# Kernel optimization log

Hardware: AMD Instinct MI355X
Metric: run time of the kernel (lower is better)

Reference implementation:

```python
import jax, jax.numpy as jnp
import numpy as np

NF, D, H = 32, 256, 128  # n_features, d_model, d_model//2
B, T = 16, 512
EPS = 1e-5

def _ln(x, g, b):
    m = jnp.mean(x, axis=-1, keepdims=True)
    v = jnp.mean((x - m) ** 2, axis=-1, keepdims=True)
    return (x - m) * jax.lax.rsqrt(v + EPS) * g + b


def setup_inputs() -> dict:
    key = jax.random.key(0)
    ks = jax.random.split(key, 16)
    s = 0.05
    inp = {
        "x": jax.random.normal(ks[0], (B, T, NF), dtype=jnp.float32),
        # batched per-feature GRN params (d_in=1 -> fc1 weight is (NF,H))
        "w1": jax.random.normal(ks[1], (NF, H)) * s,
        "b1": jnp.zeros((NF, H)),
        "w2": jax.random.normal(ks[2], (NF, H, D)) * s,
        "b2": jnp.zeros((NF, D)),
        "wg": jax.random.normal(ks[3], (NF, H, D)) * s,
        "bg": jnp.zeros((NF, D)),
        "ws": jax.random.normal(ks[4], (NF, D)) * s,  # skip Linear(1,D)
        "bs": jnp.zeros((NF, D)),
        "ln_g": jnp.ones((NF, D)),
        "ln_b": jnp.zeros((NF, D)),
        # weight GRN: d_in=NF*D, d_hidden=D, d_out=NF
        "W1": jax.random.normal(ks[5], (NF * D, D)) * s,
        "B1": jnp.zeros((D,)),
        "W2": jax.random.normal(ks[6], (D, NF)) * s,
        "B2": jnp.zeros((NF,)),
        "Wg": jax.random.normal(ks[7], (D, NF)) * s,
        "Bg": jnp.zeros((NF,)),
        "Ws": jax.random.normal(ks[8], (NF * D, NF)) * s,
        "Bs": jnp.zeros((NF,)),
        "LN_g": jnp.ones((NF,)),
        "LN_b": jnp.zeros((NF,)),
    }
    return inp


def reference(x, w1, b1, w2, b2, wg, bg, ws, bs, ln_g, ln_b,
              W1, B1, W2, B2, Wg, Bg, Ws, Bs, LN_g, LN_b):
    Bn, Tn, Fn = x.shape
    # --- all per-feature GRNs batched over the feature axis (dropout=eval/identity) ---
    h = jax.nn.elu(x[..., None] * w1 + b1)                      # (B,T,F,H)
    proj = jnp.einsum('btfh,fhd->btfd', h, w2) + b2             # (B,T,F,D)
    gate = jax.nn.sigmoid(jnp.einsum('btfh,fhd->btfd', h, wg) + bg)
    skip = x[..., None] * ws + bs                               # (B,T,F,D)
    stacked = _ln(skip + gate * proj, ln_g, ln_b)               # (B,T,F,D)
    # --- softmax feature weights from mean-pooled flat features ---
    flat_pooled = stacked.mean(axis=1).reshape(Bn, Fn * stacked.shape[-1])  # (B,F*D)
    hw = jax.nn.elu(flat_pooled @ W1 + B1)                      # (B,D)
    pw = hw @ W2 + B2
    gw = jax.nn.sigmoid(hw @ Wg + Bg)
    wgrn = _ln(flat_pooled @ Ws + Bs + gw * pw, LN_g, LN_b)     # (B,F)
    weights = jax.nn.softmax(wgrn, axis=-1)                     # (B,F)
    # --- weighted feature combine ---
    selected = jnp.einsum('btfd,bf->btd', stacked, weights)     # (B,T,D)
    return selected, weights
```

## Files before the change

kernel.cpp:

```cpp
#include <hip/hip_runtime.h>
#include <hip/hip_fp16.h>

#define NF 32
#define DM 256
#define HH 128
#define BB 16
#define TT 512
#define BT 8192
#define OUT_W_OFF 2097152
#define EPS 1e-5f

typedef __bf16 bf16x8 __attribute__((ext_vector_type(8)));
typedef float  f32x16 __attribute__((ext_vector_type(16)));
typedef __fp16 f16x2 __attribute__((ext_vector_type(2)));
typedef __fp16 f16x8 __attribute__((ext_vector_type(8)));

__device__ __forceinline__ float eluf(float z){ return z > 0.f ? z : __expf(z) - 1.f; }
__device__ __forceinline__ float sigm(float z){ return 1.f/(1.f + __expf(-z)); }
__device__ __forceinline__ unsigned f2bf(float x){
  unsigned u = __float_as_uint(x);
  u += 0x7fffu + ((u>>16)&1u);
  return u>>16;
}
__device__ __forceinline__ float rdlane(float v, int l){
  return __uint_as_float(__builtin_amdgcn_readlane(__float_as_uint(v), l));
}
__device__ __forceinline__ float qsel(float v, int mb, int lane){
  float a0 = rdlane(v, mb), a1 = rdlane(v, mb+4);
  return (lane & 32) ? a1 : a0;
}

template<int MT>
__device__ __forceinline__ void build_A(uint4* Apack, const float* __restrict__ x,
                                        const float* __restrict__ w1, const float* __restrict__ b1,
                                        int f, int tok0, int tid){
  #pragma unroll
  for (int p = 0; p < MT*2; ++p){
    int slot = tid + p*256;
    int l  = slot & 63;
    int ks = (slot>>6)&7;
    int mt = slot>>9;
    int m  = mt*32 + (l&31);
    int k0 = ks*16 + (l>>5)*8;
    float xv = x[(tok0+m)*NF + f];
    const float* wp = w1 + f*HH + k0;
    const float* bp = b1 + f*HH + k0;
    float4 wa = *(const float4*)wp, wb = *(const float4*)(wp+4);
    float4 ba = *(const float4*)bp, bb = *(const float4*)(bp+4);
    float h0 = eluf(fmaf(xv, wa.x, ba.x));
    float h1 = eluf(fmaf(xv, wa.y, ba.y));
    float h2 = eluf(fmaf(xv, wa.z, ba.z));
    float h3 = eluf(fmaf(xv, wa.w, ba.w));
    float h4 = eluf(fmaf(xv, wb.x, bb.x));
    float h5 = eluf(fmaf(xv, wb.y, bb.y));
    float h6 = eluf(fmaf(xv, wb.z, bb.z));
    float h7 = eluf(fmaf(xv, wb.w, bb.w));
    uint4 pk;
    pk.x = f2bf(h0) | (f2bf(h1)<<16);
    pk.y = f2bf(h2) | (f2bf(h3)<<16);
    pk.z = f2bf(h4) | (f2bf(h5)<<16);
    pk.w = f2bf(h6) | (f2bf(h7)<<16);
    Apack[slot] = pk;
  }
}

__global__ __launch_bounds__(256) void k_prep(const float* __restrict__ w2,
                                              const float* __restrict__ wgm,
                                              uint4* __restrict__ Wpk){
  __shared__ float ssrc[2][128][32];
  const int tid = threadIdx.x;
  const int f = blockIdx.x, c = blockIdx.y;
  #pragma unroll
  for (int it = 0; it < 32; ++it){
    int idx = tid + it*256;
    int arr = idx >> 12;
    int rem = idx & 4095;
    int k = rem >> 5, dd = rem & 31;
    const float* src = arr ? wgm : w2;
    ssrc[arr][k][dd] = src[(f*HH + k)*DM + c*32 + dd];
  }
  __syncthreads();
  #pragma unroll
  for (int p = 0; p < 4; ++p){
    int oc = tid + p*256;
    int nt = oc>>9, ks = (oc>>6)&7, l = oc&63;
    int k0 = ks*16 + (l>>5)*8, dd = l&31;
    float v[8];
    #pragma unroll
    for (int j=0;j<8;++j) v[j] = ssrc[nt][k0+j][dd];
    uint4 pk;
    pk.x = f2bf(v[0]) | (f2bf(v[1])<<16);
    pk.y = f2bf(v[2]) | (f2bf(v[3])<<16);
    pk.z = f2bf(v[4]) | (f2bf(v[5])<<16);
    pk.w = f2bf(v[6]) | (f2bf(v[7])<<16);
    Wpk[(f*8 + c)*1024 + oc] = pk;
  }
}

__global__ __launch_bounds__(256) void k_pass1(const float* __restrict__ x,  const float* __restrict__ w1,
    const float* __restrict__ b1, const float* __restrict__ b2, const float* __restrict__ bg,
    const float* __restrict__ wsk, const float* __restrict__ bsk,
    const float* __restrict__ lng, const float* __restrict__ lnb,
    const uint4* __restrict__ Wpk,
    float* __restrict__ pooled, uint4* __restrict__ stk4){
  __shared__ uint4 smem[4096];
  __shared__ float muL[128], rsL[128];
  __shared__ float poolbuf[256];
  const int tid = threadIdx.x, lane = tid&63, wid = tid>>6;
  const int col = lane&31, q = lane>>5;
  const int f = blockIdx.y;
  const int tok0 = blockIdx.x*128;
  const int b = tok0 >> 9;
  poolbuf[tid] = 0.f;
  build_A<4>(smem, x, w1, b1, f, tok0, tid);
  __syncthreads();
  bf16x8 afr[8];
  #pragma unroll
  for (int ks=0; ks<8; ++ks) afr[ks] = __builtin_bit_cast(bf16x8, smem[(wid*8+ks)*64 + lane]);
  float xl = x[(tok0 + wid*32 + col)*NF + f];
  float xr[16];
  #pragma unroll
  for (int r=0;r<16;++r) xr[r] = qsel(xl, (r&3)+8*(r>>2), lane);
  __syncthreads();
  __fp16* stage = (__fp16*)smem;
  float sum[16], ssq[16];
  #pragma unroll
  for (int r=0;r<16;++r){ sum[r]=0.f; ssq[r]=0.f; }
  for (int c=0; c<8; ++c){
    const uint4* wb = Wpk + (f*8 + c)*1024;
    bf16x8 bf0[8], bf1[8];
    #pragma unroll
    for (int ks=0;ks<8;++ks) bf0[ks] = __builtin_bit_cast(bf16x8, wb[ks*64 + lane]);
    #pragma unroll
    for (int ks=0;ks<8;++ks) bf1[ks] = __builtin_bit_cast(bf16x8, wb[512 + ks*64 + lane]);
    f32x16 acc0 = {0.f}, acc1 = {0.f};
    #pragma unroll
    for (int ks=0;ks<8;++ks){
      acc0 = __builtin_amdgcn_mfma_f32_32x32x16_bf16(afr[ks], bf0[ks], acc0, 0,0,0);
      acc1 = __builtin_amdgcn_mfma_f32_32x32x16_bf16(afr[ks], bf1[ks], acc1, 0,0,0);
    }
    const int d = c*32 + col;
    const float b2v = b2[f*DM+d], bgv = bg[f*DM+d];
    const float wsv = wsk[f*DM+d], bsv = bsk[f*DM+d];
    #pragma unroll
    for (int i=0;i<8;++i){
      const int r0 = 2*i, r1 = 2*i+1;
      const int m0 = (r0&3) + 8*(i>>1) + 4*q;
      const int t0 = wid*32 + m0;
      float sv0 = fmaf(xr[r0], wsv, bsv) + sigm(acc1[r0]+bgv)*(acc0[r0]+b2v);
      float sv1 = fmaf(xr[r1], wsv, bsv) + sigm(acc1[r1]+bgv)*(acc0[r1]+b2v);
      sum[r0] += sv0; ssq[r0] = fmaf(sv0, sv0, ssq[r0]);
      sum[r1] += sv1; ssq[r1] = fmaf(sv1, sv1, ssq[r1]);
      stage[ t0   *256 + d] = (__fp16)sv0;
      stage[(t0+1)*256 + d] = (__fp16)sv1;
    }
  }
  #pragma unroll
  for (int r=0;r<16;++r){
    float s1 = sum[r], s2 = ssq[r];
    s1 += __shfl_xor(s1,1);  s2 += __shfl_xor(s2,1);
    s1 += __shfl_xor(s1,2);  s2 += __shfl_xor(s2,2);
    s1 += __shfl_xor(s1,4);  s2 += __shfl_xor(s2,4);
    s1 += __shfl_xor(s1,8);  s2 += __shfl_xor(s2,8);
    s1 += __shfl_xor(s1,16); s2 += __shfl_xor(s2,16);
    float mu = s1 * (1.f/256.f);
    float var = fmaf(-mu, mu, s2*(1.f/256.f));
    sum[r] = mu;
    ssq[r] = rsqrtf(fmaxf(var, 0.f) + EPS);
  }
  if (col == 0){
    #pragma unroll
    for (int r=0;r<16;++r){
      int m = (r&3) + 8*(r>>2) + 4*q;
      muL[wid*32 + m] = sum[r];
      rsL[wid*32 + m] = ssq[r];
    }
  }
  __syncthreads();
  const int oc = tid & 31;
  float4 ga = *(const float4*)(lng + f*DM + oc*8);
  float4 gb = *(const float4*)(lng + f*DM + oc*8 + 4);
  float4 ba = *(const float4*)(lnb + f*DM + oc*8);
  float4 bb = *(const float4*)(lnb + f*DM + oc*8 + 4);
  float gj[8] = {ga.x,ga.y,ga.z,ga.w,gb.x,gb.y,gb.z,gb.w};
  float bj[8] = {ba.x,ba.y,ba.z,ba.w,bb.x,bb.y,bb.z,bb.w};
  float ps[8];
  #pragma unroll
  for (int j=0;j<8;++j) ps[j]=0.f;
  #pragma unroll
  for (int p=0;p<16;++p){
    int slot = tid + p*256;
    int t = slot >> 5;
    uint4 v = smem[slot];
    f16x8 s8 = __builtin_bit_cast(f16x8, v);
    float mu = muL[t], rs = rsL[t];
    float nmr = -mu*rs;
    float sh[8];
    #pragma unroll
    for (int j=0;j<8;++j){
      sh[j] = fmaf(fmaf((float)s8[j], rs, nmr), gj[j], bj[j]);
      ps[j] += sh[j];
    }
    uint4 pk;
    pk.x = __builtin_bit_cast(unsigned, __builtin_amdgcn_cvt_pkrtz(sh[0], sh[1]));
    pk.y = __builtin_bit_cast(unsigned, __builtin_amdgcn_cvt_pkrtz(sh[2], sh[3]));
    pk.z = __builtin_bit_cast(unsigned, __builtin_amdgcn_cvt_pkrtz(sh[4], sh[5]));
    pk.w = __builtin_bit_cast(unsigned, __builtin_amdgcn_cvt_pkrtz(sh[6], sh[7]));
    stk4[(size_t)f*262144 + (size_t)(tok0 + t)*32 + oc] = pk;
  }
  #pragma unroll
  for (int j=0;j<8;++j) atomicAdd(&poolbuf[oc*8 + j], ps[j]);
  __syncthreads();
  atomicAdd(&pooled[b*8192 + f*DM + tid], poolbuf[tid]);
}

__global__ __launch_bounds__(256) void k_pass2a(const float* __restrict__ pooled,
    const float* __restrict__ W1, const float* __restrict__ Wsm,
    float* __restrict__ hw_pre, float* __restrict__ sk_pre){
  __shared__ float fl[512];
  const int tid = threadIdx.x;
  const int b = blockIdx.x;
  const int k0 = blockIdx.y * 512;
  fl[tid]       = pooled[b*8192 + k0 + tid]       * (1.f/512.f);
  fl[tid+256]   = pooled[b*8192 + k0 + tid + 256] * (1.f/512.f);
  __syncthreads();
  float acc = 0.f;
  const float* wcol = W1 + (size_t)k0*DM + tid;
  #pragma unroll 4
  for (int i=0;i<512;++i) acc = fmaf(fl[i], wcol[(size_t)i*DM], acc);
  atomicAdd(&hw_pre[b*DM + tid], acc);
  const int colj = tid & 31, sub = tid >> 5;
  float acc2 = 0.f;
  const float* wscol = Wsm + (size_t)(k0 + sub*64)*NF + colj;
  const float* fls = fl + sub*64;
  #pragma unroll 4
  for (int i=0;i<64;++i) acc2 = fmaf(fls[i], wscol[(size_t)i*NF], acc2);
  atomicAdd(&sk_pre[b*NF + colj], acc2);
}

__global__ __launch_bounds__(64) void k_pass2b(const float* __restrict__ hw_pre, const float* __restrict__ sk_pre,
    const float* __restrict__ B1, const float* __restrict__ W2, const float* __restrict__ B2,
    const float* __restrict__ Wg, const float* __restrict__ Bg, const float* __restrict__ Bs,
    const float* __restrict__ LNg, const float* __restrict__ LNb,
    float* __restrict__ out, float* __restrict__ wsel){
  __shared__ float hw[256];
  const int tid = threadIdx.x, b = blockIdx.x;
  for (int i=tid;i<256;i+=64) hw[i] = eluf(hw_pre[b*DM+i] + B1[i]);
  __syncthreads();
  if (tid < 32){
    const int j = tid;
    float ap = B2[j], ag = Bg[j];
    #pragma unroll 4
    for (int i=0;i<256;++i){ float h = hw[i]; ap = fmaf(h, W2[i*NF+j], ap); ag = fmaf(h, Wg[i*NF+j], ag); }
    float gw = sigm(ag);
    float v = sk_pre[b*NF+j] + Bs[j] + gw*ap;
    float s1 = v;
    s1 += __shfl_xor(s1,1); s1 += __shfl_xor(s1,2); s1 += __shfl_xor(s1,4); s1 += __shfl_xor(s1,8); s1 += __shfl_xor(s1,16);
    float mean = s1*(1.f/32.f);
    float dv = v - mean;
    float s2 = dv*dv;
    s2 += __shfl_xor(s2,1); s2 += __shfl_xor(s2,2); s2 += __shfl_xor(s2,4); s2 += __shfl_xor(s2,8); s2 += __shfl_xor(s2,16);
    float wn = fmaf(dv * rsqrtf(s2*(1.f/32.f) + EPS), LNg[j], LNb[j]);
    float mx = wn;
    mx = fmaxf(mx, __shfl_xor(mx,1)); mx = fmaxf(mx, __shfl_xor(mx,2)); mx = fmaxf(mx, __shfl_xor(mx,4));
    mx = fmaxf(mx, __shfl_xor(mx,8)); mx = fmaxf(mx, __shfl_xor(mx,16));
    float e = __expf(wn - mx);
    float se = e;
    se += __shfl_xor(se,1); se += __shfl_xor(se,2); se += __shfl_xor(se,4); se += __shfl_xor(se,8); se += __shfl_xor(se,16);
    float wgt = e / se;
    out[OUT_W_OFF + b*NF + j] = wgt;
    wsel[b*NF + j] = wgt;
  }
}

__global__ __launch_bounds__(256) void k_comb(const uint4* __restrict__ stk4,
    const float* __restrict__ wsel, float* __restrict__ out){
  __shared__ float wloc[NF];
  const int tid = threadIdx.x, lane = tid&63;
  const int t = blockIdx.x*4 + (tid>>6);
  const int b = t >> 9;
  if (tid < NF) wloc[tid] = wsel[b*NF + tid];
  __syncthreads();
  const int oc = lane&31, fh = lane>>5;
  float acc[8];
  #pragma unroll
  for (int j=0;j<8;++j) acc[j]=0.f;
  #pragma unroll
  for (int j=0;j<16;++j){
    int f = fh*16 + j;
    uint4 v = stk4[(size_t)f*262144 + (size_t)t*32 + oc];
    f16x8 hv = __builtin_bit_cast(f16x8, v);
    float wf = wloc[f];
    #pragma unroll
    for (int jj=0;jj<8;++jj) acc[jj] = fmaf(wf, (float)hv[jj], acc[jj]);
  }
  #pragma unroll
  for (int jj=0;jj<8;++jj) acc[jj] += __shfl_xor(acc[jj], 32);
  if (fh == 0){
    float4* o = (float4*)(out + (size_t)t*DM + oc*8);
    o[0] = make_float4(acc[0],acc[1],acc[2],acc[3]);
    o[1] = make_float4(acc[4],acc[5],acc[6],acc[7]);
  }
}

extern "C" void kernel_launch(void* const* d_in, const int* in_sizes, int n_in,
                              void* d_out, int out_size, void* d_ws, size_t ws_size,
                              hipStream_t stream) {
  const float* x   = (const float*)d_in[0];
  const float* w1  = (const float*)d_in[1];
  const float* b1  = (const float*)d_in[2];
  const float* w2  = (const float*)d_in[3];
  const float* b2  = (const float*)d_in[4];
  const float* wgm = (const float*)d_in[5];
  const float* bg  = (const float*)d_in[6];
  const float* wsk = (const float*)d_in[7];
  const float* bsk = (const float*)d_in[8];
  const float* lng = (const float*)d_in[9];
  const float* lnb = (const float*)d_in[10];
  const float* W1  = (const float*)d_in[11];
  const float* B1  = (const float*)d_in[12];
  const float* W2  = (const float*)d_in[13];
  const float* B2  = (const float*)d_in[14];
  const float* Wg  = (const float*)d_in[15];
  const float* Bg  = (const float*)d_in[16];
  const float* Wsm = (const float*)d_in[17];
  const float* Bs  = (const float*)d_in[18];
  const float* LNg = (const float*)d_in[19];
  const float* LNb = (const float*)d_in[20];
  float* out = (float*)d_out;

  char* ws = (char*)d_ws;
  uint4* Wpk    = (uint4*)ws;
  uint4* stk4   = (uint4*)(ws + 4194304);
  float* pooled = (float*)(ws + 138412032);
  float* hw_pre = (float*)(ws + 138936320);
  float* sk_pre = (float*)(ws + 138952704);
  float* wsel   = (float*)(ws + 138954752);

  (void)hipMemsetAsync(pooled, 0, 524288, stream);
  (void)hipMemsetAsync(hw_pre, 0, 16384 + 2048, stream);

  k_prep<<<dim3(32,8), 256, 0, stream>>>(w2, wgm, Wpk);
  k_pass1<<<dim3(64,32), 256, 0, stream>>>(x, w1, b1, b2, bg, wsk, bsk, lng, lnb,
                                           Wpk, pooled, stk4);
  k_pass2a<<<dim3(16,16), 256, 0, stream>>>(pooled, W1, Wsm, hw_pre, sk_pre);
  k_pass2b<<<16, 64, 0, stream>>>(hw_pre, sk_pre, B1, W2, B2, Wg, Bg, Bs, LNg, LNb, out, wsel);
  k_comb<<<2048, 256, 0, stream>>>(stk4, wsel, out);
}
```

Measured before the change: 321.0 us.

## Store un-normalized pre-LN values and defer LayerNorm into pooling and combine

k_pass1 now builds the ELU hidden fragments directly in registers instead of staging them through shared memory. It writes raw pre-LayerNorm fp16 values straight to global memory in MFMA fragment order, along with per-token mean and rstd arrays. Pooling is computed algebraically from these raw values plus the statistics, removing the shared-memory LN pass and its extra syncs. k_comb applies gamma, beta, mean and rstd on the fly while reducing over features, at the cost of more per-element arithmetic, a shared-memory transpose and a more complex fragment-order layout.

```diff
diff --git a/kernel.cpp b/kernel.cpp
--- a/kernel.cpp
+++ b/kernel.cpp
@@ -30,40 +30,6 @@
   return (lane & 32) ? a1 : a0;
 }
 
-template<int MT>
-__device__ __forceinline__ void build_A(uint4* Apack, const float* __restrict__ x,
-                                        const float* __restrict__ w1, const float* __restrict__ b1,
-                                        int f, int tok0, int tid){
-  #pragma unroll
-  for (int p = 0; p < MT*2; ++p){
-    int slot = tid + p*256;
-    int l  = slot & 63;
-    int ks = (slot>>6)&7;
-    int mt = slot>>9;
-    int m  = mt*32 + (l&31);
-    int k0 = ks*16 + (l>>5)*8;
-    float xv = x[(tok0+m)*NF + f];
-    const float* wp = w1 + f*HH + k0;
-    const float* bp = b1 + f*HH + k0;
-    float4 wa = *(const float4*)wp, wb = *(const float4*)(wp+4);
-    float4 ba = *(const float4*)bp, bb = *(const float4*)(bp+4);
-    float h0 = eluf(fmaf(xv, wa.x, ba.x));
-    float h1 = eluf(fmaf(xv, wa.y, ba.y));
-    float h2 = eluf(fmaf(xv, wa.z, ba.z));
-    float h3 = eluf(fmaf(xv, wa.w, ba.w));
-    float h4 = eluf(fmaf(xv, wb.x, bb.x));
-    float h5 = eluf(fmaf(xv, wb.y, bb.y));
-    float h6 = eluf(fmaf(xv, wb.z, bb.z));
-    float h7 = eluf(fmaf(xv, wb.w, bb.w));
-    uint4 pk;
-    pk.x = f2bf(h0) | (f2bf(h1)<<16);
-    pk.y = f2bf(h2) | (f2bf(h3)<<16);
-    pk.z = f2bf(h4) | (f2bf(h5)<<16);
-    pk.w = f2bf(h6) | (f2bf(h7)<<16);
-    Apack[slot] = pk;
-  }
-}
-
 __global__ __launch_bounds__(256) void k_prep(const float* __restrict__ w2,
                                               const float* __restrict__ wgm,
                                               uint4* __restrict__ Wpk){
@@ -97,42 +63,66 @@
   }
 }
 
-__global__ __launch_bounds__(256) void k_pass1(const float* __restrict__ x,  const float* __restrict__ w1,
-    const float* __restrict__ b1, const float* __restrict__ b2, const float* __restrict__ bg,
+__global__ __launch_bounds__(256) void k_pass1(
+    const float* __restrict__ x,  const float* __restrict__ w1, const float* __restrict__ b1,
+    const float* __restrict__ b2, const float* __restrict__ bg,
     const float* __restrict__ wsk, const float* __restrict__ bsk,
     const float* __restrict__ lng, const float* __restrict__ lnb,
     const uint4* __restrict__ Wpk,
+    float* __restrict__ muw, float* __restrict__ rsw,
     float* __restrict__ pooled, uint4* __restrict__ stk4){
-  __shared__ uint4 smem[4096];
-  __shared__ float muL[128], rsL[128];
   __shared__ float poolbuf[256];
+  __shared__ float Cbuf;
   const int tid = threadIdx.x, lane = tid&63, wid = tid>>6;
   const int col = lane&31, q = lane>>5;
   const int f = blockIdx.y;
   const int tok0 = blockIdx.x*128;
   const int b = tok0 >> 9;
   poolbuf[tid] = 0.f;
-  build_A<4>(smem, x, w1, b1, f, tok0, tid);
-  __syncthreads();
+  if (tid == 0) Cbuf = 0.f;
+  __syncthreads();
+  const float xl = x[(tok0 + wid*32 + col)*NF + f];
   bf16x8 afr[8];
-  #pragma unroll
-  for (int ks=0; ks<8; ++ks) afr[ks] = __builtin_bit_cast(bf16x8, smem[(wid*8+ks)*64 + lane]);
-  float xl = x[(tok0 + wid*32 + col)*NF + f];
+  {
+    const float* wp = w1 + f*HH + q*8;
+    const float* bp = b1 + f*HH + q*8;
+    #pragma unroll
+    for (int ks=0;ks<8;++ks){
+      float4 wa = *(const float4*)(wp + ks*16);
+      float4 wb = *(const float4*)(wp + ks*16 + 4);
+      float4 ba = *(const float4*)(bp + ks*16);
+      float4 bb = *(const float4*)(bp + ks*16 + 4);
+      float h0 = eluf(fmaf(xl, wa.x, ba.x));
+      float h1 = eluf(fmaf(xl, wa.y, ba.y));
+      float h2 = eluf(fmaf(xl, wa.z, ba.z));
+      float h3 = eluf(fmaf(xl, wa.w, ba.w));
+      float h4 = eluf(fmaf(xl, wb.x, bb.x));
+      float h5 = eluf(fmaf(xl, wb.y, bb.y));
+      float h6 = eluf(fmaf(xl, wb.z, bb.z));
+      float h7 = eluf(fmaf(xl, wb.w, bb.w));
+      uint4 pk;
+      pk.x = f2bf(h0) | (f2bf(h1)<<16);
+      pk.y = f2bf(h2) | (f2bf(h3)<<16);
+      pk.z = f2bf(h4) | (f2bf(h5)<<16);
+      pk.w = f2bf(h6) | (f2bf(h7)<<16);
+      afr[ks] = __builtin_bit_cast(bf16x8, pk);
+    }
+  }
   float xr[16];
   #pragma unroll
   for (int r=0;r<16;++r) xr[r] = qsel(xl, (r&3)+8*(r>>2), lane);
-  __syncthreads();
-  __fp16* stage = (__fp16*)smem;
   float sum[16], ssq[16];
   #pragma unroll
   for (int r=0;r<16;++r){ sum[r]=0.f; ssq[r]=0.f; }
+  const size_t sbase = (size_t)f*262144 + (size_t)blockIdx.x*4096
+                     + (size_t)(wid*128 + q*64 + col*2);
   for (int c=0; c<8; ++c){
-    const uint4* wb = Wpk + (f*8 + c)*1024;
+    const uint4* wb4 = Wpk + (f*8 + c)*1024;
     bf16x8 bf0[8], bf1[8];
     #pragma unroll
-    for (int ks=0;ks<8;++ks) bf0[ks] = __builtin_bit_cast(bf16x8, wb[ks*64 + lane]);
-    #pragma unroll
-    for (int ks=0;ks<8;++ks) bf1[ks] = __builtin_bit_cast(bf16x8, wb[512 + ks*64 + lane]);
+    for (int ks=0;ks<8;++ks) bf0[ks] = __builtin_bit_cast(bf16x8, wb4[ks*64 + lane]);
+    #pragma unroll
+    for (int ks=0;ks<8;++ks) bf1[ks] = __builtin_bit_cast(bf16x8, wb4[512 + ks*64 + lane]);
     f32x16 acc0 = {0.f}, acc1 = {0.f};
     #pragma unroll
     for (int ks=0;ks<8;++ks){
@@ -142,18 +132,21 @@
     const int d = c*32 + col;
     const float b2v = b2[f*DM+d], bgv = bg[f*DM+d];
     const float wsv = wsk[f*DM+d], bsv = bsk[f*DM+d];
+    unsigned pk[8];
     #pragma unroll
     for (int i=0;i<8;++i){
       const int r0 = 2*i, r1 = 2*i+1;
-      const int m0 = (r0&3) + 8*(i>>1) + 4*q;
-      const int t0 = wid*32 + m0;
       float sv0 = fmaf(xr[r0], wsv, bsv) + sigm(acc1[r0]+bgv)*(acc0[r0]+b2v);
       float sv1 = fmaf(xr[r1], wsv, bsv) + sigm(acc1[r1]+bgv)*(acc0[r1]+b2v);
       sum[r0] += sv0; ssq[r0] = fmaf(sv0, sv0, ssq[r0]);
       sum[r1] += sv1; ssq[r1] = fmaf(sv1, sv1, ssq[r1]);
-      stage[ t0   *256 + d] = (__fp16)sv0;
-      stage[(t0+1)*256 + d] = (__fp16)sv1;
-    }
+      pk[i] = __builtin_bit_cast(unsigned, __builtin_amdgcn_cvt_pkrtz(sv0, sv1));
+    }
+    uint4 u0, u1;
+    u0.x = pk[0]; u0.y = pk[1]; u0.z = pk[2]; u0.w = pk[3];
+    u1.x = pk[4]; u1.y = pk[5]; u1.z = pk[6]; u1.w = pk[7];
+    stk4[sbase + c*512    ] = u0;
+    stk4[sbase + c*512 + 1] = u1;
   }
   #pragma unroll
   for (int r=0;r<16;++r){
@@ -169,49 +162,37 @@
     ssq[r] = rsqrtf(fmaxf(var, 0.f) + EPS);
   }
   if (col == 0){
-    #pragma unroll
-    for (int r=0;r<16;++r){
-      int m = (r&3) + 8*(r>>2) + 4*q;
-      muL[wid*32 + m] = sum[r];
-      rsL[wid*32 + m] = ssq[r];
-    }
-  }
-  __syncthreads();
-  const int oc = tid & 31;
-  float4 ga = *(const float4*)(lng + f*DM + oc*8);
-  float4 gb = *(const float4*)(lng + f*DM + oc*8 + 4);
-  float4 ba = *(const float4*)(lnb + f*DM + oc*8);
-  float4 bb = *(const float4*)(lnb + f*DM + oc*8 + 4);
-  float gj[8] = {ga.x,ga.y,ga.z,ga.w,gb.x,gb.y,gb.z,gb.w};
-  float bj[8] = {ba.x,ba.y,ba.z,ba.w,bb.x,bb.y,bb.z,bb.w};
-  float ps[8];
-  #pragma unroll
-  for (int j=0;j<8;++j) ps[j]=0.f;
-  #pragma unroll
-  for (int p=0;p<16;++p){
-    int slot = tid + p*256;
-    int t = slot >> 5;
-    uint4 v = smem[slot];
-    f16x8 s8 = __builtin_bit_cast(f16x8, v);
-    float mu = muL[t], rs = rsL[t];
-    float nmr = -mu*rs;
-    float sh[8];
-    #pragma unroll
-    for (int j=0;j<8;++j){
-      sh[j] = fmaf(fmaf((float)s8[j], rs, nmr), gj[j], bj[j]);
-      ps[j] += sh[j];
-    }
-    uint4 pk;
-    pk.x = __builtin_bit_cast(unsigned, __builtin_amdgcn_cvt_pkrtz(sh[0], sh[1]));
-    pk.y = __builtin_bit_cast(unsigned, __builtin_amdgcn_cvt_pkrtz(sh[2], sh[3]));
-    pk.z = __builtin_bit_cast(unsigned, __builtin_amdgcn_cvt_pkrtz(sh[4], sh[5]));
-    pk.w = __builtin_bit_cast(unsigned, __builtin_amdgcn_cvt_pkrtz(sh[6], sh[7]));
-    stk4[(size_t)f*262144 + (size_t)(tok0 + t)*32 + oc] = pk;
-  }
-  #pragma unroll
-  for (int j=0;j<8;++j) atomicAdd(&poolbuf[oc*8 + j], ps[j]);
-  __syncthreads();
-  atomicAdd(&pooled[b*8192 + f*DM + tid], poolbuf[tid]);
+    const int tb = tok0 + wid*32 + 4*q;
+    *(float4*)(muw + f*BT + tb)      = make_float4(sum[0],sum[1],sum[2],sum[3]);
+    *(float4*)(muw + f*BT + tb + 8)  = make_float4(sum[4],sum[5],sum[6],sum[7]);
+    *(float4*)(muw + f*BT + tb + 16) = make_float4(sum[8],sum[9],sum[10],sum[11]);
+    *(float4*)(muw + f*BT + tb + 24) = make_float4(sum[12],sum[13],sum[14],sum[15]);
+    *(float4*)(rsw + f*BT + tb)      = make_float4(ssq[0],ssq[1],ssq[2],ssq[3]);
+    *(float4*)(rsw + f*BT + tb + 8)  = make_float4(ssq[4],ssq[5],ssq[6],ssq[7]);
+    *(float4*)(rsw + f*BT + tb + 16) = make_float4(ssq[8],ssq[9],ssq[10],ssq[11]);
+    *(float4*)(rsw + f*BT + tb + 24) = make_float4(ssq[12],ssq[13],ssq[14],ssq[15]);
+  }
+  float Cpart = 0.f;
+  #pragma unroll
+  for (int r=0;r<16;++r) Cpart = fmaf(sum[r], ssq[r], Cpart);
+  #pragma unroll
+  for (int c=0;c<8;++c){
+    uint4 u0 = stk4[sbase + c*512];
+    uint4 u1 = stk4[sbase + c*512 + 1];
+    f16x8 a = __builtin_bit_cast(f16x8, u0);
+    f16x8 g = __builtin_bit_cast(f16x8, u1);
+    float A = 0.f;
+    #pragma unroll
+    for (int jj=0;jj<8;++jj) A = fmaf((float)a[jj], ssq[jj], A);
+    #pragma unroll
+    for (int jj=0;jj<8;++jj) A = fmaf((float)g[jj], ssq[8+jj], A);
+    A += __shfl_xor(A, 32);
+    if (q == 0) atomicAdd(&poolbuf[c*32 + col], A);
+  }
+  if (col == 0) atomicAdd(&Cbuf, Cpart);
+  __syncthreads();
+  const float contrib = fmaf(lng[f*DM+tid], poolbuf[tid] - Cbuf, 128.f*lnb[f*DM+tid]);
+  atomicAdd(&pooled[b*8192 + f*DM + tid], contrib);
 }
 
 __global__ __launch_bounds__(256) void k_pass2a(const float* __restrict__ pooled,
@@ -274,32 +255,74 @@
 }
 
 __global__ __launch_bounds__(256) void k_comb(const uint4* __restrict__ stk4,
-    const float* __restrict__ wsel, float* __restrict__ out){
-  __shared__ float wloc[NF];
-  const int tid = threadIdx.x, lane = tid&63;
-  const int t = blockIdx.x*4 + (tid>>6);
-  const int b = t >> 9;
-  if (tid < NF) wloc[tid] = wsel[b*NF + tid];
-  __syncthreads();
-  const int oc = lane&31, fh = lane>>5;
-  float acc[8];
-  #pragma unroll
-  for (int j=0;j<8;++j) acc[j]=0.f;
-  #pragma unroll
-  for (int j=0;j<16;++j){
-    int f = fh*16 + j;
-    uint4 v = stk4[(size_t)f*262144 + (size_t)t*32 + oc];
-    f16x8 hv = __builtin_bit_cast(f16x8, v);
-    float wf = wloc[f];
-    #pragma unroll
-    for (int jj=0;jj<8;++jj) acc[jj] = fmaf(wf, (float)hv[jj], acc[jj]);
-  }
-  #pragma unroll
-  for (int jj=0;jj<8;++jj) acc[jj] += __shfl_xor(acc[jj], 32);
-  if (fh == 0){
-    float4* o = (float4*)(out + (size_t)t*DM + oc*8);
-    o[0] = make_float4(acc[0],acc[1],acc[2],acc[3]);
-    o[1] = make_float4(acc[4],acc[5],acc[6],acc[7]);
+    const float* __restrict__ muw, const float* __restrict__ rsw,
+    const float* __restrict__ wsel, const float* __restrict__ lng, const float* __restrict__ lnb,
+    float* __restrict__ out){
+  __shared__ float A1L[NF*16];
+  __shared__ float MUL[NF*16];
+  __shared__ float wLs[NF];
+  __shared__ float obuf[16*256];
+  const int tid = threadIdx.x;
+  const int bi = blockIdx.x;
+  const int blk = bi>>3, wid = (bi>>1)&3, q = bi&1;
+  const int tokw = blk*128 + wid*32;
+  const int b = blk>>2;
+  if (tid < NF) wLs[tid] = wsel[b*NF + tid];
+  for (int e = tid; e < NF*16; e += 256){
+    const int fe = e>>4, r = e&15;
+    const int m = (r&3) + 8*(r>>2) + 4*q;
+    const float rs = rsw[fe*BT + tokw + m];
+    A1L[e] = wsel[b*NF + fe] * rs;
+    MUL[e] = muw[fe*BT + tokw + m];
+  }
+  __syncthreads();
+  const int U1 = tid + 256;
+  const int c0 = tid>>6, j0 = tid&63, col0 = (j0>>1)&31, h0 = j0&1;
+  const int c1 = U1>>6,  j1 = U1&63,  col1 = (j1>>1)&31, h1 = j1&1;
+  const size_t base = (size_t)blk*4096 + (size_t)(wid*128 + q*64);
+  const size_t o0 = base + c0*512 + col0*2 + h0;
+  const size_t o1 = base + c1*512 + col1*2 + h1;
+  const int d0 = c0*32+col0, d1 = c1*32+col1;
+  float acc0[8], acc1[8], accW0 = 0.f, accW1 = 0.f;
+  #pragma unroll
+  for (int jj=0;jj<8;++jj){ acc0[jj]=0.f; acc1[jj]=0.f; }
+  for (int f=0; f<NF; ++f){
+    const size_t fo = (size_t)f*262144;
+    uint4 v0 = stk4[fo + o0];
+    uint4 v1 = stk4[fo + o1];
+    float g0 = lng[f*DM+d0], bv0 = lnb[f*DM+d0];
+    float g1 = lng[f*DM+d1], bv1 = lnb[f*DM+d1];
+    float wf = wLs[f];
+    accW0 = fmaf(wf, bv0, accW0);
+    accW1 = fmaf(wf, bv1, accW1);
+    f16x8 s0 = __builtin_bit_cast(f16x8, v0);
+    f16x8 s1 = __builtin_bit_cast(f16x8, v1);
+    #pragma unroll
+    for (int jj=0;jj<8;++jj){
+      float A1 = A1L[f*16 + h0*8 + jj];
+      float mu = MUL[f*16 + h0*8 + jj];
+      acc0[jj] = fmaf(g0*A1, (float)s0[jj] - mu, acc0[jj]);
+    }
+    #pragma unroll
+    for (int jj=0;jj<8;++jj){
+      float A1 = A1L[f*16 + h1*8 + jj];
+      float mu = MUL[f*16 + h1*8 + jj];
+      acc1[jj] = fmaf(g1*A1, (float)s1[jj] - mu, acc1[jj]);
+    }
+  }
+  #pragma unroll
+  for (int jj=0;jj<8;++jj){
+    obuf[(h0*8+jj)*256 + d0] = acc0[jj] + accW0;
+    obuf[(h1*8+jj)*256 + d1] = acc1[jj] + accW1;
+  }
+  __syncthreads();
+  const float4* ob4 = (const float4*)obuf;
+  #pragma unroll
+  for (int p=0;p<4;++p){
+    int L = tid + 256*p;
+    int r = L>>6, rest = L&63;
+    int m = (r&3) + 8*(r>>2) + 4*q;
+    *(float4*)(out + (size_t)(tokw+m)*DM + rest*4) = ob4[L];
   }
 }
 
@@ -332,18 +355,20 @@
   char* ws = (char*)d_ws;
   uint4* Wpk    = (uint4*)ws;
   uint4* stk4   = (uint4*)(ws + 4194304);
-  float* pooled = (float*)(ws + 138412032);
-  float* hw_pre = (float*)(ws + 138936320);
-  float* sk_pre = (float*)(ws + 138952704);
-  float* wsel   = (float*)(ws + 138954752);
+  float* muw    = (float*)(ws + 138412032);
+  float* rsw    = (float*)(ws + 139460608);
+  float* pooled = (float*)(ws + 140509184);
+  float* hw_pre = (float*)(ws + 141033472);
+  float* sk_pre = (float*)(ws + 141049856);
+  float* wsel   = (float*)(ws + 141051904);
 
   (void)hipMemsetAsync(pooled, 0, 524288, stream);
   (void)hipMemsetAsync(hw_pre, 0, 16384 + 2048, stream);
 
   k_prep<<<dim3(32,8), 256, 0, stream>>>(w2, wgm, Wpk);
   k_pass1<<<dim3(64,32), 256, 0, stream>>>(x, w1, b1, b2, bg, wsk, bsk, lng, lnb,
-                                           Wpk, pooled, stk4);
+                                           Wpk, muw, rsw, pooled, stk4);
   k_pass2a<<<dim3(16,16), 256, 0, stream>>>(pooled, W1, Wsm, hw_pre, sk_pre);
   k_pass2b<<<16, 64, 0, stream>>>(hw_pre, sk_pre, B1, W2, B2, Wg, Bg, Bs, LNg, LNb, out, wsel);
-  k_comb<<<2048, 256, 0, stream>>>(stk4, wsel, out);
-}
+  k_comb<<<512, 256, 0, stream>>>(stk4, muw, rsw, wsel, lng, lnb, out);
+}
```

New measurement: 329.2 us. 1.03x slower.
